# Performance work log

Measured on AMD Instinct MI355X. Metric: run time of the kernel, lower is better.

The kernel has to match this reference:

```python
import jax, jax.numpy as jnp
import numpy as np

B, T, D, H = 8, 1024, 1024, 16
NEG = -1e9  # stands in for -inf in the causal mask (matches float('-inf') semantics under softmax)


def setup_inputs() -> dict:
    key = jax.random.key(0)
    ks = jax.random.split(key, 8)
    s = 0.02
    x = jax.random.normal(ks[0], (B, T, D), dtype=jnp.float32)
    # additive causal mask like whisper: zeros on/below diagonal, -inf above
    mask = jnp.triu(jnp.full((T, T), NEG, dtype=jnp.float32), k=1)
    Wq = jax.random.normal(ks[1], (D, D), dtype=jnp.float32) * s
    bq = jax.random.normal(ks[2], (D,), dtype=jnp.float32) * s
    Wk = jax.random.normal(ks[3], (D, D), dtype=jnp.float32) * s
    Wv = jax.random.normal(ks[4], (D, D), dtype=jnp.float32) * s
    bv = jax.random.normal(ks[5], (D,), dtype=jnp.float32) * s
    Wo = jax.random.normal(ks[6], (D, D), dtype=jnp.float32) * s
    bo = jax.random.normal(ks[7], (D,), dtype=jnp.float32) * s
    return {"x": x, "mask": mask, "Wq": Wq, "bq": bq, "Wk": Wk, "Wv": Wv, "bv": bv, "Wo": Wo, "bo": bo}


def reference(x, mask, Wq, bq, Wk, Wv, bv, Wo, bo):
    n_batch, n_ctx, n_state = x.shape
    head_dim = n_state // H
    scale = head_dim ** (-0.25)

    q = x @ Wq.T + bq            # [B,T,D]
    k = x @ Wk.T                 # key Linear has no bias
    v = x @ Wv.T + bv

    # [B,T,D] -> [B,H,T,hd]
    q = q.reshape(n_batch, n_ctx, H, head_dim).transpose(0, 2, 1, 3) * scale
    kt = k.reshape(n_batch, n_ctx, H, head_dim).transpose(0, 2, 3, 1) * scale  # [B,H,hd,T]
    v = v.reshape(n_batch, n_ctx, H, head_dim).transpose(0, 2, 1, 3)

    qk = jnp.einsum('bhqd,bhdk->bhqk', q, kt) + mask[:n_ctx, :n_ctx]
    w = jax.nn.softmax(qk.astype(jnp.float32), axis=-1).astype(q.dtype)
    wv = jnp.einsum('bhqk,bhkd->bhqd', w, v)  # [B,H,T,hd]
    wv = wv.transpose(0, 2, 1, 3).reshape(n_batch, n_ctx, n_state)
    return wv @ Wo.T + bo
```

## Files before the change

### kernel.cpp

```cpp
#include <hip/hip_runtime.h>
#include <stdint.h>

typedef unsigned short u16;
typedef __attribute__((ext_vector_type(8))) short bf16x8;
typedef __attribute__((ext_vector_type(4))) float f32x4;

__device__ __forceinline__ float b2f(u16 u) {
    union { uint32_t i; float f; } c; c.i = ((uint32_t)u) << 16; return c.f;
}
__device__ __forceinline__ u16 f2b(float f) {
    union { float f; uint32_t i; } c; c.f = f;
    uint32_t u = c.i;
    uint32_t r = (u + 0x7fffu + ((u >> 16) & 1u)) >> 16;
    return (u16)r;
}
__device__ __forceinline__ uint32_t fbits(float f) {
    union { float f; uint32_t u; } c; c.f = f; return c.u;
}

__device__ __forceinline__ void gll16(const u16* g, u16* lds_base) {
    __builtin_amdgcn_global_load_lds(
        (const __attribute__((address_space(1))) uint32_t*)g,
        (__attribute__((address_space(3))) uint32_t*)lds_base, 16, 0, 0);
}

#define GK 1024
#define QSCALE 0.18033688011112042f
#define LDPA 72

__global__ __launch_bounds__(256) void conv_all(
    const void* x, const void* wq, const void* bqp, const void* wk,
    const void* wv, const void* bvp, const void* wo, const void* bop,
    u16* xb, u16* wqb, u16* bqb, u16* wkb, u16* wvb, u16* bvb, u16* wob, u16* bob,
    const u16* __restrict__ sniff)
{
    const bool is_f32 = (sniff[1] == 0);
    const int blk = blockIdx.x;
    const void* s; u16* d; int i0, n;
    if (blk < 4096)      { s = x;   d = xb;  i0 = blk;        n = 8388608; }
    else if (blk < 4608) { s = wq;  d = wqb; i0 = blk - 4096; n = 1048576; }
    else if (blk < 5120) { s = wk;  d = wkb; i0 = blk - 4608; n = 1048576; }
    else if (blk < 5632) { s = wv;  d = wvb; i0 = blk - 5120; n = 1048576; }
    else if (blk < 6144) { s = wo;  d = wob; i0 = blk - 5632; n = 1048576; }
    else if (blk == 6144){ s = bqp; d = bqb; i0 = 0;          n = 1024; }
    else if (blk == 6145){ s = bvp; d = bvb; i0 = 0;          n = 1024; }
    else                 { s = bop; d = bob; i0 = 0;          n = 1024; }
    int i = (i0 * 256 + threadIdx.x) * 8;
    if (i >= n) return;
    if (is_f32) {
        const float* sf = (const float*)s;
        float4 lo = *(const float4*)(sf + i);
        float4 hi = *(const float4*)(sf + i + 4);
        u16 o[8];
        o[0]=f2b(lo.x); o[1]=f2b(lo.y); o[2]=f2b(lo.z); o[3]=f2b(lo.w);
        o[4]=f2b(hi.x); o[5]=f2b(hi.y); o[6]=f2b(hi.z); o[7]=f2b(hi.w);
        *(uint4*)(d + i) = *(const uint4*)o;
    } else {
        *(uint4*)(d + i) = *(const uint4*)((const u16*)s + i);
    }
}

__global__ __launch_bounds__(256) void gemm_qkv(
    const u16* __restrict__ xb,
    const u16* __restrict__ wq, const u16* __restrict__ wk, const u16* __restrict__ wv,
    const u16* __restrict__ bq, const u16* __restrict__ bv,
    u16* __restrict__ qb, u16* __restrict__ kb, u16* __restrict__ vtb)
{
    __shared__ __align__(16) u16 As[128 * 64];
    __shared__ __align__(16) u16 Bs[128 * 64];

    const int flat = blockIdx.x;
    const int xcd = flat & 7, pos = flat >> 3;
    const int m0 = (xcd * 8 + (pos & 7)) * 128;
    const int nb = pos >> 3;
    const int which = nb >> 3;
    const int n0 = (nb & 7) * 128;
    const u16* W = (which == 0) ? wq : (which == 1) ? wk : wv;

    const int t = threadIdx.x;
    const int lane = t & 63, w = t >> 6;
    const int quad = lane >> 4, l15 = lane & 15;
    const int wm = (w >> 1) * 64, wn = (w & 1) * 64;
    const int srow = (lane >> 3), scol = (lane & 7) * 8;

    f32x4 acc[4][4];
#pragma unroll
    for (int i = 0; i < 4; i++)
#pragma unroll
        for (int j = 0; j < 4; j++)
            acc[i][j] = (f32x4){0.f, 0.f, 0.f, 0.f};

    for (int kk = 0; kk < GK / 64; kk++) {
        const int k0 = kk * 64;
        __syncthreads();
#pragma unroll
        for (int i = 0; i < 4; i++) {
            const int rbase = w * 32 + i * 8;
            gll16(xb + (size_t)(m0 + rbase + srow) * GK + k0 + scol, &As[rbase * 64]);
            gll16(W  + (size_t)(n0 + rbase + srow) * GK + k0 + scol, &Bs[rbase * 64]);
        }
        __syncthreads();
#pragma unroll
        for (int ks = 0; ks < 2; ks++) {
            bf16x8 af[4], bfr[4];
#pragma unroll
            for (int mi = 0; mi < 4; mi++)
                af[mi] = *(const bf16x8*)(&As[(wm + mi * 16 + l15) * 64 + ks * 32 + quad * 8]);
#pragma unroll
            for (int ni = 0; ni < 4; ni++)
                bfr[ni] = *(const bf16x8*)(&Bs[(wn + ni * 16 + l15) * 64 + ks * 32 + quad * 8]);
#pragma unroll
            for (int mi = 0; mi < 4; mi++)
#pragma unroll
                for (int ni = 0; ni < 4; ni++)
                    acc[mi][ni] = __builtin_amdgcn_mfma_f32_16x16x32_bf16(
                        af[mi], bfr[ni], acc[mi][ni], 0, 0, 0);
        }
    }

#pragma unroll
    for (int mi = 0; mi < 4; mi++)
#pragma unroll
        for (int ni = 0; ni < 4; ni++) {
            int gn = n0 + wn + ni * 16 + l15;
            if (which == 2) {
                int gmb = m0 + wm + mi * 16 + quad * 4;
                int b = gmb >> 10, ml = gmb & 1023;
                int h = gn >> 6, dw = gn & 63;
                union { u16 h4[4]; uint2 v; } pk;
#pragma unroll
                for (int r = 0; r < 4; r++)
                    pk.h4[r] = f2b(acc[mi][ni][r] + b2f(bv[gn]));
                *(uint2*)(vtb + (((size_t)(b * 16 + h) * 64 + dw) << 10) + ml) = pk.v;
            } else if (which == 0) {
                float bb = b2f(bq[gn]);
#pragma unroll
                for (int r = 0; r < 4; r++) {
                    int gm = m0 + wm + mi * 16 + quad * 4 + r;
                    qb[(size_t)gm * 1024 + gn] = f2b((acc[mi][ni][r] + bb) * QSCALE);
                }
            } else {
#pragma unroll
                for (int r = 0; r < 4; r++) {
                    int gm = m0 + wm + mi * 16 + quad * 4 + r;
                    kb[(size_t)gm * 1024 + gn] = f2b(acc[mi][ni][r]);
                }
            }
        }
}

__global__ __launch_bounds__(256) void gemm_out(
    const u16* __restrict__ A, const u16* __restrict__ W,
    const u16* __restrict__ bias, float* __restrict__ C)
{
    __shared__ __align__(16) u16 As[128 * 64];
    __shared__ __align__(16) u16 Bs[128 * 64];

    const int flat = blockIdx.x;
    const int xcd = flat & 7, pos = flat >> 3;
    const int m0 = (xcd * 8 + (pos & 7)) * 128;
    const int n0 = (pos >> 3) * 128;

    const int t = threadIdx.x;
    const int lane = t & 63, w = t >> 6;
    const int quad = lane >> 4, l15 = lane & 15;
    const int wm = (w >> 1) * 64, wn = (w & 1) * 64;
    const int srow = (lane >> 3), scol = (lane & 7) * 8;

    f32x4 acc[4][4];
#pragma unroll
    for (int i = 0; i < 4; i++)
#pragma unroll
        for (int j = 0; j < 4; j++)
            acc[i][j] = (f32x4){0.f, 0.f, 0.f, 0.f};

    for (int kk = 0; kk < GK / 64; kk++) {
        const int k0 = kk * 64;
        __syncthreads();
#pragma unroll
        for (int i = 0; i < 4; i++) {
            const int rbase = w * 32 + i * 8;
            gll16(A + (size_t)(m0 + rbase + srow) * GK + k0 + scol, &As[rbase * 64]);
            gll16(W + (size_t)(n0 + rbase + srow) * GK + k0 + scol, &Bs[rbase * 64]);
        }
        __syncthreads();
#pragma unroll
        for (int ks = 0; ks < 2; ks++) {
            bf16x8 af[4], bfr[4];
#pragma unroll
            for (int mi = 0; mi < 4; mi++)
                af[mi] = *(const bf16x8*)(&As[(wm + mi * 16 + l15) * 64 + ks * 32 + quad * 8]);
#pragma unroll
            for (int ni = 0; ni < 4; ni++)
                bfr[ni] = *(const bf16x8*)(&Bs[(wn + ni * 16 + l15) * 64 + ks * 32 + quad * 8]);
#pragma unroll
            for (int mi = 0; mi < 4; mi++)
#pragma unroll
                for (int ni = 0; ni < 4; ni++)
                    acc[mi][ni] = __builtin_amdgcn_mfma_f32_16x16x32_bf16(
                        af[mi], bfr[ni], acc[mi][ni], 0, 0, 0);
        }
    }

#pragma unroll
    for (int mi = 0; mi < 4; mi++)
#pragma unroll
        for (int ni = 0; ni < 4; ni++) {
            int gn = n0 + wn + ni * 16 + l15;
            float bb = b2f(bias[gn]);
#pragma unroll
            for (int r = 0; r < 4; r++) {
                int gm = m0 + wm + mi * 16 + quad * 4 + r;
                C[(size_t)gm * 1024 + gn] = acc[mi][ni][r] + bb;
            }
        }
}

__global__ __launch_bounds__(512, 4) void attn_kernel(
    const u16* q, const u16* kg, const u16* vt, u16* o)
{
    const int qt = (blockIdx.x + 2 * (blockIdx.y >> 6)) & 3;
    const int bh = blockIdx.y;
    const int b = bh >> 4, h = bh & 15;
    const size_t base = (size_t)b * 1024 * 1024 + (size_t)h * 64;
    const size_t vbase = (size_t)bh * 64 * 1024;

    __shared__ __align__(16) u16 Ks[2][64 * LDPA];
    __shared__ __align__(16) u16 Vs[2][64 * LDPA];
    __shared__ __align__(16) u16 U[256 * LDPA];

    const int t = threadIdx.x;
    const int lane = t & 63, w = t >> 6;
    const int quad = lane >> 4, l15 = lane & 15;

#pragma unroll
    for (int i = 0; i < 4; i++) {
        int idx = i * 512 + t;
        int r = idx >> 3, c = idx & 7;
        *(uint4*)(&U[r * LDPA + c * 8]) =
            *(const uint4*)(q + base + (size_t)(qt * 256 + r) * 1024 + c * 8);
    }
    __syncthreads();
    bf16x8 qf[2][2];
#pragma unroll
    for (int qc = 0; qc < 2; qc++)
#pragma unroll
        for (int ks = 0; ks < 2; ks++)
            qf[qc][ks] = *(const bf16x8*)(&U[(w * 32 + qc * 16 + l15) * LDPA + ks * 32 + quad * 8]);
    __syncthreads();
    u16* Pw = &U[(w * 32) * LDPA];

    const int wqmin = qt * 256 + w * 32;
    float l_[2] = {0.f, 0.f};
    f32x4 accO[2][4];
#pragma unroll
    for (int qc = 0; qc < 2; qc++)
#pragma unroll
        for (int f = 0; f < 4; f++) accO[qc][f] = (f32x4){0.f, 0.f, 0.f, 0.f};

    const int jmax = 4 * qt + 3;
    const int sr = t >> 3, sc = (t & 7) * 8;
    uint4 rK = *(const uint4*)(kg + base + (size_t)sr * 1024 + sc);
    uint4 rV = *(const uint4*)(vt + vbase + (size_t)sr * 1024 + sc);

    for (int j = 0; j <= jmax; j++) {
        const int buf = j & 1;
        *(uint4*)(&Ks[buf][sr * LDPA + sc]) = rK;
        *(uint4*)(&Vs[buf][sr * LDPA + sc]) = rV;
        if (j < jmax) {
            rK = *(const uint4*)(kg + base + (size_t)((j + 1) * 64 + sr) * 1024 + sc);
            rV = *(const uint4*)(vt + vbase + (size_t)sr * 1024 + (j + 1) * 64 + sc);
        }
        __syncthreads();

        if (j * 64 > wqmin + 31) continue;

        f32x4 st[2][4];
#pragma unroll
        for (int qc = 0; qc < 2; qc++)
#pragma unroll
            for (int ni = 0; ni < 4; ni++) st[qc][ni] = (f32x4){0.f, 0.f, 0.f, 0.f};
#pragma unroll
        for (int ks = 0; ks < 2; ks++)
#pragma unroll
            for (int ni = 0; ni < 4; ni++) {
                bf16x8 kf = *(const bf16x8*)(&Ks[buf][(ni * 16 + l15) * LDPA + ks * 32 + quad * 8]);
                st[0][ni] = __builtin_amdgcn_mfma_f32_16x16x32_bf16(kf, qf[0][ks], st[0][ni], 0, 0, 0);
                st[1][ni] = __builtin_amdgcn_mfma_f32_16x16x32_bf16(kf, qf[1][ks], st[1][ni], 0, 0, 0);
            }

        const bool diag = (j * 64 + 63 > wqmin);
#pragma unroll
        for (int qc = 0; qc < 2; qc++) {
            const int q_g = wqmin + qc * 16 + l15;
            float ps = 0.f;
#pragma unroll
            for (int ni = 0; ni < 4; ni++) {
                float p[4];
#pragma unroll
                for (int r = 0; r < 4; r++) {
                    float e = __builtin_amdgcn_exp2f(st[qc][ni][r]);
                    if (diag) {
                        int key_g = j * 64 + ni * 16 + quad * 4 + r;
                        e = (key_g > q_g) ? 0.f : e;
                    }
                    p[r] = e;
                    ps += e;
                }
                uint2 pkv;
                pkv.x = __builtin_amdgcn_perm(fbits(p[1]) + 0x8000u, fbits(p[0]) + 0x8000u, 0x07060302u);
                pkv.y = __builtin_amdgcn_perm(fbits(p[3]) + 0x8000u, fbits(p[2]) + 0x8000u, 0x07060302u);
                *(uint2*)(&Pw[(qc * 16 + l15) * LDPA + ni * 16 + quad * 4]) = pkv;
            }
            l_[qc] += ps;
        }

#pragma unroll
        for (int ks = 0; ks < 2; ks++) {
            bf16x8 pf0 = *(const bf16x8*)(&Pw[(l15) * LDPA + ks * 32 + quad * 8]);
            bf16x8 pf1 = *(const bf16x8*)(&Pw[(16 + l15) * LDPA + ks * 32 + quad * 8]);
#pragma unroll
            for (int f = 0; f < 4; f++) {
                bf16x8 vf = *(const bf16x8*)(&Vs[buf][(f * 16 + l15) * LDPA + ks * 32 + quad * 8]);
                accO[0][f] = __builtin_amdgcn_mfma_f32_16x16x32_bf16(vf, pf0, accO[0][f], 0, 0, 0);
                accO[1][f] = __builtin_amdgcn_mfma_f32_16x16x32_bf16(vf, pf1, accO[1][f], 0, 0, 0);
            }
        }
    }

#pragma unroll
    for (int qc = 0; qc < 2; qc++) {
        float l = l_[qc];
        l += __shfl_xor(l, 16, 64);
        l += __shfl_xor(l, 32, 64);
        float inv = 1.0f / l;
        const int q_g = wqmin + qc * 16 + l15;
#pragma unroll
        for (int f = 0; f < 4; f++) {
            union { u16 h4[4]; uint2 v; } pk;
#pragma unroll
            for (int r = 0; r < 4; r++) pk.h4[r] = f2b(accO[qc][f][r] * inv);
            *(uint2*)(o + base + (size_t)q_g * 1024 + f * 16 + quad * 4) = pk.v;
        }
    }
}

extern "C" void kernel_launch(void* const* d_in, const int* in_sizes, int n_in,
                              void* d_out, int out_size, void* d_ws, size_t ws_size,
                              hipStream_t stream) {
    const u16* mask = (const u16*)d_in[1];

    const size_t MT = (size_t)8192 * 1024;
    const size_t WT = (size_t)1024 * 1024;
    u16* ws  = (u16*)d_ws;
    u16* xb  = ws;
    u16* qb  = xb + MT;
    u16* kb  = qb + MT;
    u16* vtb = kb + MT;
    u16* wqb = vtb + MT;
    u16* wkb = wqb + WT;
    u16* wvb = wkb + WT;
    u16* wob = wvb + WT;
    u16* bqb = wob + WT;
    u16* bvb = bqb + 1024;
    u16* bob = bvb + 1024;

    hipLaunchKernelGGL(conv_all, dim3(6147), dim3(256), 0, stream,
                       d_in[0], d_in[2], d_in[3], d_in[4], d_in[5], d_in[6],
                       d_in[7], d_in[8],
                       xb, wqb, bqb, wkb, wvb, bvb, wob, bob, mask);

    hipLaunchKernelGGL(gemm_qkv, dim3(1536), dim3(256), 0, stream,
                       xb, wqb, wkb, wvb, bqb, bvb, qb, kb, vtb);

    hipLaunchKernelGGL(attn_kernel, dim3(4, 128), dim3(512), 0, stream, qb, kb, vtb, qb);

    hipLaunchKernelGGL(gemm_out, dim3(512), dim3(256), 0, stream,
                       qb, wob, bob, (float*)d_out);
}
```

Baseline: 256.4 us.

## Rewrite projection GEMMs with 256x256 tiles and 4-stage async LDS pipeline

Both projection GEMMs move from 128x128 tiles with a synchronous load/compute loop to 256x256 tiles on 512-thread blocks. Each K-slice of 32 goes through a 4-slot LDS ring, so global-to-LDS loads of later tiles overlap the MFMA work on the current one. LDS rows use an XOR swizzle to avoid bank conflicts, and MFMA sections get raised wave priority. The QKV GEMM reads the three weights as one contiguous combined matrix, relying on wq/wk/wv being adjacent in the workspace. The larger tiles cut operand reloads, but they give fewer blocks (384 and 128), which may underfill the CUs.

After: 277.1 us. 1.08x slower.

```diff
diff --git a/kernel.cpp b/kernel.cpp
--- a/kernel.cpp
+++ b/kernel.cpp
@@ -60,159 +60,235 @@
     }
 }
 
-__global__ __launch_bounds__(256) void gemm_qkv(
-    const u16* __restrict__ xb,
-    const u16* __restrict__ wq, const u16* __restrict__ wk, const u16* __restrict__ wv,
+
+__global__ __launch_bounds__(512, 2) void gemm_qkv(
+    const u16* __restrict__ xb, const u16* __restrict__ wcomb,
     const u16* __restrict__ bq, const u16* __restrict__ bv,
     u16* __restrict__ qb, u16* __restrict__ kb, u16* __restrict__ vtb)
 {
-    __shared__ __align__(16) u16 As[128 * 64];
-    __shared__ __align__(16) u16 Bs[128 * 64];
+    __shared__ __align__(16) u16 As[4][256 * 32];
+    __shared__ __align__(16) u16 Bs[4][256 * 32];
 
     const int flat = blockIdx.x;
-    const int xcd = flat & 7, pos = flat >> 3;
-    const int m0 = (xcd * 8 + (pos & 7)) * 128;
-    const int nb = pos >> 3;
-    const int which = nb >> 3;
-    const int n0 = (nb & 7) * 128;
-    const u16* W = (which == 0) ? wq : (which == 1) ? wk : wv;
+    const int swz = (flat & 7) * 48 + (flat >> 3);
+    const int mt = swz / 12, nt = swz % 12;
+    const int m0 = mt * 256;
+    const int n0full = nt * 256;
 
     const int t = threadIdx.x;
     const int lane = t & 63, w = t >> 6;
     const int quad = lane >> 4, l15 = lane & 15;
-    const int wm = (w >> 1) * 64, wn = (w & 1) * 64;
-    const int srow = (lane >> 3), scol = (lane & 7) * 8;
-
-    f32x4 acc[4][4];
-#pragma unroll
-    for (int i = 0; i < 4; i++)
-#pragma unroll
-        for (int j = 0; j < 4; j++)
-            acc[i][j] = (f32x4){0.f, 0.f, 0.f, 0.f};
-
-    for (int kk = 0; kk < GK / 64; kk++) {
-        const int k0 = kk * 64;
-        __syncthreads();
-#pragma unroll
-        for (int i = 0; i < 4; i++) {
-            const int rbase = w * 32 + i * 8;
-            gll16(xb + (size_t)(m0 + rbase + srow) * GK + k0 + scol, &As[rbase * 64]);
-            gll16(W  + (size_t)(n0 + rbase + srow) * GK + k0 + scol, &Bs[rbase * 64]);
-        }
-        __syncthreads();
-#pragma unroll
-        for (int ks = 0; ks < 2; ks++) {
-            bf16x8 af[4], bfr[4];
-#pragma unroll
-            for (int mi = 0; mi < 4; mi++)
-                af[mi] = *(const bf16x8*)(&As[(wm + mi * 16 + l15) * 64 + ks * 32 + quad * 8]);
+    const int wm = w >> 2, wn = w & 3;
+
+    const int r0 = (w * 128 + lane) >> 2;
+    const int g0 = (lane & 3) ^ (r0 & 3);
+    const int r1 = (w * 128 + 64 + lane) >> 2;
+    const int g1 = (lane & 3) ^ (r1 & 3);
+    const u16* srcA0 = xb    + (size_t)(m0 + r0) * GK + g0 * 8;
+    const u16* srcA1 = xb    + (size_t)(m0 + r1) * GK + g1 * 8;
+    const u16* srcB0 = wcomb + (size_t)(n0full + r0) * GK + g0 * 8;
+    const u16* srcB1 = wcomb + (size_t)(n0full + r1) * GK + g1 * 8;
+
+    const int sq = ((quad ^ (l15 & 3))) * 8;
+    int offA[8], offB[4];
+#pragma unroll
+    for (int mi = 0; mi < 8; mi++)
+        offA[mi] = (wm * 128 + mi * 16 + l15) * 32 + sq;
+#pragma unroll
+    for (int ni = 0; ni < 4; ni++)
+        offB[ni] = (wn * 64 + ni * 16 + l15) * 32 + sq;
+
+    f32x4 acc[8][4];
+#pragma unroll
+    for (int mi = 0; mi < 8; mi++)
+#pragma unroll
+        for (int ni = 0; ni < 4; ni++)
+            acc[mi][ni] = (f32x4){0.f, 0.f, 0.f, 0.f};
+
+    auto STAGE = [&](int tile) {
+        const int slot = tile & 3;
+        const int ko = tile * 32;
+        u16* la = &As[slot][w * 1024];
+        u16* lb = &Bs[slot][w * 1024];
+        gll16(srcA0 + ko, la);
+        gll16(srcA1 + ko, la + 512);
+        gll16(srcB0 + ko, lb);
+        gll16(srcB1 + ko, lb + 512);
+    };
+    auto COMPUTE = [&](int tile) {
+        const int slot = tile & 3;
+        const u16* as = &As[slot][0];
+        const u16* bs = &Bs[slot][0];
+        bf16x8 af[8], bf[4];
+#pragma unroll
+        for (int mi = 0; mi < 8; mi++) af[mi] = *(const bf16x8*)(as + offA[mi]);
+#pragma unroll
+        for (int ni = 0; ni < 4; ni++) bf[ni] = *(const bf16x8*)(bs + offB[ni]);
+        __builtin_amdgcn_s_setprio(1);
+#pragma unroll
+        for (int mi = 0; mi < 8; mi++)
 #pragma unroll
             for (int ni = 0; ni < 4; ni++)
-                bfr[ni] = *(const bf16x8*)(&Bs[(wn + ni * 16 + l15) * 64 + ks * 32 + quad * 8]);
-#pragma unroll
-            for (int mi = 0; mi < 4; mi++)
-#pragma unroll
-                for (int ni = 0; ni < 4; ni++)
-                    acc[mi][ni] = __builtin_amdgcn_mfma_f32_16x16x32_bf16(
-                        af[mi], bfr[ni], acc[mi][ni], 0, 0, 0);
-        }
-    }
-
-#pragma unroll
-    for (int mi = 0; mi < 4; mi++)
+                acc[mi][ni] = __builtin_amdgcn_mfma_f32_16x16x32_bf16(
+                    af[mi], bf[ni], acc[mi][ni], 0, 0, 0);
+        __builtin_amdgcn_s_setprio(0);
+    };
+
+    STAGE(0); STAGE(1); STAGE(2);
+
+    for (int tt = 0; tt < 29; ++tt) {
+        asm volatile("s_waitcnt vmcnt(8) lgkmcnt(0)" ::: "memory");
+        __builtin_amdgcn_s_barrier();
+        asm volatile("" ::: "memory");
+        STAGE(tt + 3);
+        COMPUTE(tt);
+    }
+    asm volatile("s_waitcnt vmcnt(8) lgkmcnt(0)" ::: "memory");
+    __builtin_amdgcn_s_barrier();
+    asm volatile("" ::: "memory");
+    COMPUTE(29);
+    asm volatile("s_waitcnt vmcnt(4) lgkmcnt(0)" ::: "memory");
+    __builtin_amdgcn_s_barrier();
+    asm volatile("" ::: "memory");
+    COMPUTE(30);
+    asm volatile("s_waitcnt vmcnt(0) lgkmcnt(0)" ::: "memory");
+    __builtin_amdgcn_s_barrier();
+    asm volatile("" ::: "memory");
+    COMPUTE(31);
+
+    const int which = nt >> 2;
+    const int nbase = (nt & 3) * 256 + wn * 64;
+#pragma unroll
+    for (int mi = 0; mi < 8; mi++)
 #pragma unroll
         for (int ni = 0; ni < 4; ni++) {
-            int gn = n0 + wn + ni * 16 + l15;
+            const int gn = nbase + ni * 16 + l15;
+            const int gm = m0 + wm * 128 + mi * 16 + quad * 4;
             if (which == 2) {
-                int gmb = m0 + wm + mi * 16 + quad * 4;
-                int b = gmb >> 10, ml = gmb & 1023;
-                int h = gn >> 6, dw = gn & 63;
+                const int b = gm >> 10, ml = gm & 1023;
+                const int h = gn >> 6, dw = gn & 63;
+                const float bb = b2f(bv[gn]);
                 union { u16 h4[4]; uint2 v; } pk;
 #pragma unroll
                 for (int r = 0; r < 4; r++)
-                    pk.h4[r] = f2b(acc[mi][ni][r] + b2f(bv[gn]));
+                    pk.h4[r] = f2b(acc[mi][ni][r] + bb);
                 *(uint2*)(vtb + (((size_t)(b * 16 + h) * 64 + dw) << 10) + ml) = pk.v;
             } else if (which == 0) {
-                float bb = b2f(bq[gn]);
-#pragma unroll
-                for (int r = 0; r < 4; r++) {
-                    int gm = m0 + wm + mi * 16 + quad * 4 + r;
-                    qb[(size_t)gm * 1024 + gn] = f2b((acc[mi][ni][r] + bb) * QSCALE);
-                }
+                const float bb = b2f(bq[gn]);
+#pragma unroll
+                for (int r = 0; r < 4; r++)
+                    qb[(size_t)(gm + r) * 1024 + gn] = f2b((acc[mi][ni][r] + bb) * QSCALE);
             } else {
 #pragma unroll
-                for (int r = 0; r < 4; r++) {
-                    int gm = m0 + wm + mi * 16 + quad * 4 + r;
-                    kb[(size_t)gm * 1024 + gn] = f2b(acc[mi][ni][r]);
-                }
+                for (int r = 0; r < 4; r++)
+                    kb[(size_t)(gm + r) * 1024 + gn] = f2b(acc[mi][ni][r]);
             }
         }
 }
 
-__global__ __launch_bounds__(256) void gemm_out(
+__global__ __launch_bounds__(512, 2) void gemm_out(
     const u16* __restrict__ A, const u16* __restrict__ W,
     const u16* __restrict__ bias, float* __restrict__ C)
 {
-    __shared__ __align__(16) u16 As[128 * 64];
-    __shared__ __align__(16) u16 Bs[128 * 64];
+    __shared__ __align__(16) u16 As[4][256 * 32];
+    __shared__ __align__(16) u16 Bs[4][256 * 32];
 
     const int flat = blockIdx.x;
-    const int xcd = flat & 7, pos = flat >> 3;
-    const int m0 = (xcd * 8 + (pos & 7)) * 128;
-    const int n0 = (pos >> 3) * 128;
+    const int swz = (flat & 7) * 16 + (flat >> 3);
+    const int mt = swz >> 2, nt = swz & 3;
+    const int m0 = mt * 256;
+    const int n0 = nt * 256;
 
     const int t = threadIdx.x;
     const int lane = t & 63, w = t >> 6;
     const int quad = lane >> 4, l15 = lane & 15;
-    const int wm = (w >> 1) * 64, wn = (w & 1) * 64;
-    const int srow = (lane >> 3), scol = (lane & 7) * 8;
-
-    f32x4 acc[4][4];
-#pragma unroll
-    for (int i = 0; i < 4; i++)
-#pragma unroll
-        for (int j = 0; j < 4; j++)
-            acc[i][j] = (f32x4){0.f, 0.f, 0.f, 0.f};
-
-    for (int kk = 0; kk < GK / 64; kk++) {
-        const int k0 = kk * 64;
-        __syncthreads();
-#pragma unroll
-        for (int i = 0; i < 4; i++) {
-            const int rbase = w * 32 + i * 8;
-            gll16(A + (size_t)(m0 + rbase + srow) * GK + k0 + scol, &As[rbase * 64]);
-            gll16(W + (size_t)(n0 + rbase + srow) * GK + k0 + scol, &Bs[rbase * 64]);
-        }
-        __syncthreads();
-#pragma unroll
-        for (int ks = 0; ks < 2; ks++) {
-            bf16x8 af[4], bfr[4];
-#pragma unroll
-            for (int mi = 0; mi < 4; mi++)
-                af[mi] = *(const bf16x8*)(&As[(wm + mi * 16 + l15) * 64 + ks * 32 + quad * 8]);
+    const int wm = w >> 2, wn = w & 3;
+
+    const int r0 = (w * 128 + lane) >> 2;
+    const int g0 = (lane & 3) ^ (r0 & 3);
+    const int r1 = (w * 128 + 64 + lane) >> 2;
+    const int g1 = (lane & 3) ^ (r1 & 3);
+    const u16* srcA0 = A + (size_t)(m0 + r0) * GK + g0 * 8;
+    const u16* srcA1 = A + (size_t)(m0 + r1) * GK + g1 * 8;
+    const u16* srcB0 = W + (size_t)(n0 + r0) * GK + g0 * 8;
+    const u16* srcB1 = W + (size_t)(n0 + r1) * GK + g1 * 8;
+
+    const int sq = ((quad ^ (l15 & 3))) * 8;
+    int offA[8], offB[4];
+#pragma unroll
+    for (int mi = 0; mi < 8; mi++)
+        offA[mi] = (wm * 128 + mi * 16 + l15) * 32 + sq;
+#pragma unroll
+    for (int ni = 0; ni < 4; ni++)
+        offB[ni] = (wn * 64 + ni * 16 + l15) * 32 + sq;
+
+    f32x4 acc[8][4];
+#pragma unroll
+    for (int mi = 0; mi < 8; mi++)
+#pragma unroll
+        for (int ni = 0; ni < 4; ni++)
+            acc[mi][ni] = (f32x4){0.f, 0.f, 0.f, 0.f};
+
+    auto STAGE = [&](int tile) {
+        const int slot = tile & 3;
+        const int ko = tile * 32;
+        u16* la = &As[slot][w * 1024];
+        u16* lb = &Bs[slot][w * 1024];
+        gll16(srcA0 + ko, la);
+        gll16(srcA1 + ko, la + 512);
+        gll16(srcB0 + ko, lb);
+        gll16(srcB1 + ko, lb + 512);
+    };
+    auto COMPUTE = [&](int tile) {
+        const int slot = tile & 3;
+        const u16* as = &As[slot][0];
+        const u16* bs = &Bs[slot][0];
+        bf16x8 af[8], bf[4];
+#pragma unroll
+        for (int mi = 0; mi < 8; mi++) af[mi] = *(const bf16x8*)(as + offA[mi]);
+#pragma unroll
+        for (int ni = 0; ni < 4; ni++) bf[ni] = *(const bf16x8*)(bs + offB[ni]);
+        __builtin_amdgcn_s_setprio(1);
+#pragma unroll
+        for (int mi = 0; mi < 8; mi++)
 #pragma unroll
             for (int ni = 0; ni < 4; ni++)
-                bfr[ni] = *(const bf16x8*)(&Bs[(wn + ni * 16 + l15) * 64 + ks * 32 + quad * 8]);
-#pragma unroll
-            for (int mi = 0; mi < 4; mi++)
-#pragma unroll
-                for (int ni = 0; ni < 4; ni++)
-                    acc[mi][ni] = __builtin_amdgcn_mfma_f32_16x16x32_bf16(
-                        af[mi], bfr[ni], acc[mi][ni], 0, 0, 0);
-        }
-    }
-
-#pragma unroll
-    for (int mi = 0; mi < 4; mi++)
+                acc[mi][ni] = __builtin_amdgcn_mfma_f32_16x16x32_bf16(
+                    af[mi], bf[ni], acc[mi][ni], 0, 0, 0);
+        __builtin_amdgcn_s_setprio(0);
+    };
+
+    STAGE(0); STAGE(1); STAGE(2);
+    for (int tt = 0; tt < 29; ++tt) {
+        asm volatile("s_waitcnt vmcnt(8) lgkmcnt(0)" ::: "memory");
+        __builtin_amdgcn_s_barrier();
+        asm volatile("" ::: "memory");
+        STAGE(tt + 3);
+        COMPUTE(tt);
+    }
+    asm volatile("s_waitcnt vmcnt(8) lgkmcnt(0)" ::: "memory");
+    __builtin_amdgcn_s_barrier();
+    asm volatile("" ::: "memory");
+    COMPUTE(29);
+    asm volatile("s_waitcnt vmcnt(4) lgkmcnt(0)" ::: "memory");
+    __builtin_amdgcn_s_barrier();
+    asm volatile("" ::: "memory");
+    COMPUTE(30);
+    asm volatile("s_waitcnt vmcnt(0) lgkmcnt(0)" ::: "memory");
+    __builtin_amdgcn_s_barrier();
+    asm volatile("" ::: "memory");
+    COMPUTE(31);
+
+#pragma unroll
+    for (int mi = 0; mi < 8; mi++)
 #pragma unroll
         for (int ni = 0; ni < 4; ni++) {
-            int gn = n0 + wn + ni * 16 + l15;
-            float bb = b2f(bias[gn]);
-#pragma unroll
-            for (int r = 0; r < 4; r++) {
-                int gm = m0 + wm + mi * 16 + quad * 4 + r;
-                C[(size_t)gm * 1024 + gn] = acc[mi][ni][r] + bb;
-            }
+            const int gn = n0 + wn * 64 + ni * 16 + l15;
+            const int gm = m0 + wm * 128 + mi * 16 + quad * 4;
+            const float bb = b2f(bias[gn]);
+#pragma unroll
+            for (int r = 0; r < 4; r++)
+                C[(size_t)(gm + r) * 1024 + gn] = acc[mi][ni][r] + bb;
         }
 }
 
@@ -370,11 +446,11 @@
                        d_in[7], d_in[8],
                        xb, wqb, bqb, wkb, wvb, bvb, wob, bob, mask);
 
-    hipLaunchKernelGGL(gemm_qkv, dim3(1536), dim3(256), 0, stream,
-                       xb, wqb, wkb, wvb, bqb, bvb, qb, kb, vtb);
+    hipLaunchKernelGGL(gemm_qkv, dim3(384), dim3(512), 0, stream,
+                       xb, wqb, bqb, bvb, qb, kb, vtb);
 
     hipLaunchKernelGGL(attn_kernel, dim3(4, 128), dim3(512), 0, stream, qb, kb, vtb, qb);
 
-    hipLaunchKernelGGL(gemm_out, dim3(512), dim3(256), 0, stream,
+    hipLaunchKernelGGL(gemm_out, dim3(128), dim3(512), 0, stream,
                        qb, wob, bob, (float*)d_out);
 }
```

## Double-buffer LDS in QKV and output GEMMs with 128x256 tiles

Applied to the files above, without the earlier changes.

Both GEMMs now use 512-thread blocks computing 128x256 tiles. They keep two LDS buffers so the global-to-LDS loads for the next K slice are issued while MFMAs run on the current one, with one barrier per iteration. The QKV GEMM treats Wq/Wk/Wv as one combined 3072-row weight, relying on the contiguous workspace layout. MFMA sections are wrapped in setprio, and the tile swizzle is changed for XCD locality. The larger tiles and double buffering raise LDS use to 96KB per block, which may cap occupancy.

Measured after the change: 252.5 us. About the same (-1.5%).

```diff
diff --git a/kernel.cpp b/kernel.cpp
--- a/kernel.cpp
+++ b/kernel.cpp
@@ -60,28 +60,38 @@
     }
 }
 
-__global__ __launch_bounds__(256) void gemm_qkv(
-    const u16* __restrict__ xb,
-    const u16* __restrict__ wq, const u16* __restrict__ wk, const u16* __restrict__ wv,
+
+#define NGRAN 3072
+#define BOFF  8192
+
+__global__ __launch_bounds__(512, 2) void gemm_qkv(
+    const u16* __restrict__ xb, const u16* __restrict__ wcomb,
     const u16* __restrict__ bq, const u16* __restrict__ bv,
     u16* __restrict__ qb, u16* __restrict__ kb, u16* __restrict__ vtb)
 {
-    __shared__ __align__(16) u16 As[128 * 64];
-    __shared__ __align__(16) u16 Bs[128 * 64];
+    __shared__ __align__(16) u16 S[2][NGRAN * 8];
 
     const int flat = blockIdx.x;
-    const int xcd = flat & 7, pos = flat >> 3;
-    const int m0 = (xcd * 8 + (pos & 7)) * 128;
-    const int nb = pos >> 3;
-    const int which = nb >> 3;
-    const int n0 = (nb & 7) * 128;
-    const u16* W = (which == 0) ? wq : (which == 1) ? wk : wv;
+    const int swz = (flat & 7) * 96 + (flat >> 3);
+    const int mt = swz & 63, nt = swz >> 6;
+    const int m0 = mt * 128;
+    const int n0full = nt * 256;
 
     const int t = threadIdx.x;
     const int lane = t & 63, w = t >> 6;
     const int quad = lane >> 4, l15 = lane & 15;
-    const int wm = (w >> 1) * 64, wn = (w & 1) * 64;
-    const int srow = (lane >> 3), scol = (lane & 7) * 8;
+    const int wm = w >> 2, wn = w & 3;
+
+    const int srow = lane >> 3, scol = (lane & 7) * 8;
+    const u16* srcp[6];
+    int ldso[6];
+#pragma unroll
+    for (int L = 0; L < 6; L++) {
+        const int c = L * 8 + w;
+        ldso[L] = c * 512;
+        if (c < 16)  srcp[L] = xb    + (size_t)(m0 + c * 8 + srow) * GK + scol;
+        else         srcp[L] = wcomb + (size_t)(n0full + (c - 16) * 8 + srow) * GK + scol;
+    }
 
     f32x4 acc[4][4];
 #pragma unroll
@@ -90,82 +100,100 @@
         for (int j = 0; j < 4; j++)
             acc[i][j] = (f32x4){0.f, 0.f, 0.f, 0.f};
 
-    for (int kk = 0; kk < GK / 64; kk++) {
-        const int k0 = kk * 64;
-        __syncthreads();
-#pragma unroll
-        for (int i = 0; i < 4; i++) {
-            const int rbase = w * 32 + i * 8;
-            gll16(xb + (size_t)(m0 + rbase + srow) * GK + k0 + scol, &As[rbase * 64]);
-            gll16(W  + (size_t)(n0 + rbase + srow) * GK + k0 + scol, &Bs[rbase * 64]);
-        }
-        __syncthreads();
+#pragma unroll
+    for (int L = 0; L < 6; L++) gll16(srcp[L], &S[0][ldso[L]]);
+    asm volatile("s_waitcnt vmcnt(0)" ::: "memory");
+    __builtin_amdgcn_s_barrier();
+    asm volatile("" ::: "memory");
+
+    for (int tt = 0; tt < 16; ++tt) {
+        if (tt < 15) {
+            const int k0 = (tt + 1) * 64;
+            u16* Sn = &S[(tt + 1) & 1][0];
+#pragma unroll
+            for (int L = 0; L < 6; L++) gll16(srcp[L] + k0, Sn + ldso[L]);
+        }
+        const u16* Sb = &S[tt & 1][0];
 #pragma unroll
         for (int ks = 0; ks < 2; ks++) {
-            bf16x8 af[4], bfr[4];
+            bf16x8 af[4], bf[4];
 #pragma unroll
             for (int mi = 0; mi < 4; mi++)
-                af[mi] = *(const bf16x8*)(&As[(wm + mi * 16 + l15) * 64 + ks * 32 + quad * 8]);
+                af[mi] = *(const bf16x8*)(Sb + (wm * 64 + mi * 16 + l15) * 64 + ks * 32 + quad * 8);
 #pragma unroll
             for (int ni = 0; ni < 4; ni++)
-                bfr[ni] = *(const bf16x8*)(&Bs[(wn + ni * 16 + l15) * 64 + ks * 32 + quad * 8]);
+                bf[ni] = *(const bf16x8*)(Sb + BOFF + (wn * 64 + ni * 16 + l15) * 64 + ks * 32 + quad * 8);
+            __builtin_amdgcn_s_setprio(1);
 #pragma unroll
             for (int mi = 0; mi < 4; mi++)
 #pragma unroll
                 for (int ni = 0; ni < 4; ni++)
                     acc[mi][ni] = __builtin_amdgcn_mfma_f32_16x16x32_bf16(
-                        af[mi], bfr[ni], acc[mi][ni], 0, 0, 0);
-        }
-    }
-
+                        af[mi], bf[ni], acc[mi][ni], 0, 0, 0);
+            __builtin_amdgcn_s_setprio(0);
+        }
+        asm volatile("s_waitcnt vmcnt(0) lgkmcnt(0)" ::: "memory");
+        __builtin_amdgcn_s_barrier();
+        asm volatile("" ::: "memory");
+    }
+
+    const int which = nt >> 2;
+    const int nbase = (nt & 3) * 256 + wn * 64;
 #pragma unroll
     for (int mi = 0; mi < 4; mi++)
 #pragma unroll
         for (int ni = 0; ni < 4; ni++) {
-            int gn = n0 + wn + ni * 16 + l15;
+            const int gn = nbase + ni * 16 + l15;
+            const int gm = m0 + wm * 64 + mi * 16 + quad * 4;
             if (which == 2) {
-                int gmb = m0 + wm + mi * 16 + quad * 4;
-                int b = gmb >> 10, ml = gmb & 1023;
-                int h = gn >> 6, dw = gn & 63;
+                const int b = gm >> 10, ml = gm & 1023;
+                const int h = gn >> 6, dw = gn & 63;
+                const float bb = b2f(bv[gn]);
                 union { u16 h4[4]; uint2 v; } pk;
 #pragma unroll
                 for (int r = 0; r < 4; r++)
-                    pk.h4[r] = f2b(acc[mi][ni][r] + b2f(bv[gn]));
+                    pk.h4[r] = f2b(acc[mi][ni][r] + bb);
                 *(uint2*)(vtb + (((size_t)(b * 16 + h) * 64 + dw) << 10) + ml) = pk.v;
             } else if (which == 0) {
-                float bb = b2f(bq[gn]);
-#pragma unroll
-                for (int r = 0; r < 4; r++) {
-                    int gm = m0 + wm + mi * 16 + quad * 4 + r;
-                    qb[(size_t)gm * 1024 + gn] = f2b((acc[mi][ni][r] + bb) * QSCALE);
-                }
+                const float bb = b2f(bq[gn]);
+#pragma unroll
+                for (int r = 0; r < 4; r++)
+                    qb[(size_t)(gm + r) * 1024 + gn] = f2b((acc[mi][ni][r] + bb) * QSCALE);
             } else {
 #pragma unroll
-                for (int r = 0; r < 4; r++) {
-                    int gm = m0 + wm + mi * 16 + quad * 4 + r;
-                    kb[(size_t)gm * 1024 + gn] = f2b(acc[mi][ni][r]);
-                }
+                for (int r = 0; r < 4; r++)
+                    kb[(size_t)(gm + r) * 1024 + gn] = f2b(acc[mi][ni][r]);
             }
         }
 }
 
-__global__ __launch_bounds__(256) void gemm_out(
+__global__ __launch_bounds__(512, 2) void gemm_out(
     const u16* __restrict__ A, const u16* __restrict__ W,
     const u16* __restrict__ bias, float* __restrict__ C)
 {
-    __shared__ __align__(16) u16 As[128 * 64];
-    __shared__ __align__(16) u16 Bs[128 * 64];
+    __shared__ __align__(16) u16 S[2][NGRAN * 8];
 
     const int flat = blockIdx.x;
-    const int xcd = flat & 7, pos = flat >> 3;
-    const int m0 = (xcd * 8 + (pos & 7)) * 128;
-    const int n0 = (pos >> 3) * 128;
+    const int swz = (flat & 7) * 32 + (flat >> 3);
+    const int mt = swz & 63, nt = swz >> 6;
+    const int m0 = mt * 128;
+    const int n0 = nt * 256;
 
     const int t = threadIdx.x;
     const int lane = t & 63, w = t >> 6;
     const int quad = lane >> 4, l15 = lane & 15;
-    const int wm = (w >> 1) * 64, wn = (w & 1) * 64;
-    const int srow = (lane >> 3), scol = (lane & 7) * 8;
+    const int wm = w >> 2, wn = w & 3;
+
+    const int srow = lane >> 3, scol = (lane & 7) * 8;
+    const u16* srcp[6];
+    int ldso[6];
+#pragma unroll
+    for (int L = 0; L < 6; L++) {
+        const int c = L * 8 + w;
+        ldso[L] = c * 512;
+        if (c < 16)  srcp[L] = A + (size_t)(m0 + c * 8 + srow) * GK + scol;
+        else         srcp[L] = W + (size_t)(n0 + (c - 16) * 8 + srow) * GK + scol;
+    }
 
     f32x4 acc[4][4];
 #pragma unroll
@@ -174,45 +202,53 @@
         for (int j = 0; j < 4; j++)
             acc[i][j] = (f32x4){0.f, 0.f, 0.f, 0.f};
 
-    for (int kk = 0; kk < GK / 64; kk++) {
-        const int k0 = kk * 64;
-        __syncthreads();
-#pragma unroll
-        for (int i = 0; i < 4; i++) {
-            const int rbase = w * 32 + i * 8;
-            gll16(A + (size_t)(m0 + rbase + srow) * GK + k0 + scol, &As[rbase * 64]);
-            gll16(W + (size_t)(n0 + rbase + srow) * GK + k0 + scol, &Bs[rbase * 64]);
-        }
-        __syncthreads();
+#pragma unroll
+    for (int L = 0; L < 6; L++) gll16(srcp[L], &S[0][ldso[L]]);
+    asm volatile("s_waitcnt vmcnt(0)" ::: "memory");
+    __builtin_amdgcn_s_barrier();
+    asm volatile("" ::: "memory");
+
+    for (int tt = 0; tt < 16; ++tt) {
+        if (tt < 15) {
+            const int k0 = (tt + 1) * 64;
+            u16* Sn = &S[(tt + 1) & 1][0];
+#pragma unroll
+            for (int L = 0; L < 6; L++) gll16(srcp[L] + k0, Sn + ldso[L]);
+        }
+        const u16* Sb = &S[tt & 1][0];
 #pragma unroll
         for (int ks = 0; ks < 2; ks++) {
-            bf16x8 af[4], bfr[4];
+            bf16x8 af[4], bf[4];
 #pragma unroll
             for (int mi = 0; mi < 4; mi++)
-                af[mi] = *(const bf16x8*)(&As[(wm + mi * 16 + l15) * 64 + ks * 32 + quad * 8]);
+                af[mi] = *(const bf16x8*)(Sb + (wm * 64 + mi * 16 + l15) * 64 + ks * 32 + quad * 8);
 #pragma unroll
             for (int ni = 0; ni < 4; ni++)
-                bfr[ni] = *(const bf16x8*)(&Bs[(wn + ni * 16 + l15) * 64 + ks * 32 + quad * 8]);
+                bf[ni] = *(const bf16x8*)(Sb + BOFF + (wn * 64 + ni * 16 + l15) * 64 + ks * 32 + quad * 8);
+            __builtin_amdgcn_s_setprio(1);
 #pragma unroll
             for (int mi = 0; mi < 4; mi++)
 #pragma unroll
                 for (int ni = 0; ni < 4; ni++)
                     acc[mi][ni] = __builtin_amdgcn_mfma_f32_16x16x32_bf16(
-                        af[mi], bfr[ni], acc[mi][ni], 0, 0, 0);
-        }
+                        af[mi], bf[ni], acc[mi][ni], 0, 0, 0);
+            __builtin_amdgcn_s_setprio(0);
+        }
+        asm volatile("s_waitcnt vmcnt(0) lgkmcnt(0)" ::: "memory");
+        __builtin_amdgcn_s_barrier();
+        asm volatile("" ::: "memory");
     }
 
 #pragma unroll
     for (int mi = 0; mi < 4; mi++)
 #pragma unroll
         for (int ni = 0; ni < 4; ni++) {
-            int gn = n0 + wn + ni * 16 + l15;
-            float bb = b2f(bias[gn]);
-#pragma unroll
-            for (int r = 0; r < 4; r++) {
-                int gm = m0 + wm + mi * 16 + quad * 4 + r;
-                C[(size_t)gm * 1024 + gn] = acc[mi][ni][r] + bb;
-            }
+            const int gn = n0 + wn * 64 + ni * 16 + l15;
+            const int gm = m0 + wm * 64 + mi * 16 + quad * 4;
+            const float bb = b2f(bias[gn]);
+#pragma unroll
+            for (int r = 0; r < 4; r++)
+                C[(size_t)(gm + r) * 1024 + gn] = acc[mi][ni][r] + bb;
         }
 }
 
@@ -370,11 +406,11 @@
                        d_in[7], d_in[8],
                        xb, wqb, bqb, wkb, wvb, bvb, wob, bob, mask);
 
-    hipLaunchKernelGGL(gemm_qkv, dim3(1536), dim3(256), 0, stream,
-                       xb, wqb, wkb, wvb, bqb, bvb, qb, kb, vtb);
+    hipLaunchKernelGGL(gemm_qkv, dim3(768), dim3(512), 0, stream,
+                       xb, wqb, bqb, bvb, qb, kb, vtb);
 
     hipLaunchKernelGGL(attn_kernel, dim3(4, 128), dim3(512), 0, stream, qb, kb, vtb, qb);
 
-    hipLaunchKernelGGL(gemm_out, dim3(512), dim3(256), 0, stream,
+    hipLaunchKernelGGL(gemm_out, dim3(256), dim3(512), 0, stream,
                        qb, wob, bob, (float*)d_out);
 }
```
